# Optimization experiments

Measured on AMD Instinct MI355X. Metric: run time of the kernel, lower is better.

Reference implementation:

```python
import jax, jax.numpy as jnp
import numpy as np
from jax import lax

K = 10  # k_neighbors (k = min(k, N); N=1024 so k=10)


def setup_inputs() -> dict:
    key = jax.random.key(0)
    ks = jax.random.split(key, 6)
    B, N, M, D = 4, 1024, 8, 128
    PROJ, NC, OUT = 64, 10, 128
    x = jax.random.normal(ks[0], (B, N, M, D), dtype=jnp.float32)
    # Linear params (torch stores weight as [out, in])
    W_proj_w = jax.random.normal(ks[1], (PROJ, D), dtype=jnp.float32) / np.sqrt(D)
    W_proj_b = jnp.zeros((PROJ,), dtype=jnp.float32)
    C = jax.random.normal(ks[2], (NC, PROJ), dtype=jnp.float32) * np.sqrt(2.0 / (NC + PROJ))
    Theta_w = jax.random.normal(ks[3], (OUT, D), dtype=jnp.float32) / np.sqrt(D)
    Theta_b = jnp.zeros((OUT,), dtype=jnp.float32)
    return {"x": x, "W_proj_w": W_proj_w, "W_proj_b": W_proj_b, "C": C,
            "Theta_w": Theta_w, "Theta_b": Theta_b}


def _forward(x, W_proj_w, W_proj_b, C, Theta_w, Theta_b):
    B, N, M, D = x.shape
    BM = B * M
    x_flat = jnp.transpose(x, (0, 2, 1, 3)).reshape(BM, N, D)
    Z = x_flat @ W_proj_w.T + W_proj_b  # [BM, N, P]
    # squared euclidean pairwise distances (same topk ordering as cdist)
    sq = jnp.sum(Z * Z, axis=-1)  # [BM, N]
    d2 = sq[:, :, None] + sq[:, None, :] - 2.0 * jnp.einsum('bnp,bmp->bnm', Z, Z)
    _, idx = lax.top_k(-d2, K)  # k smallest distances -> [BM, N, K]
    # scatter 1.0 at neighbor indices
    b_ix = jnp.arange(BM)[:, None, None]
    r_ix = jnp.arange(N)[None, :, None]
    H_knn = jnp.zeros((BM, N, N), dtype=jnp.float32).at[b_ix, r_ix, idx].set(1.0)
    H_cluster = jax.nn.softmax(Z @ C.T, axis=-1)  # [BM, N, NC]
    H = jnp.concatenate([H_knn, H_cluster], axis=-1)  # [BM, N, N+NC]
    # hypergraph conv with degree normalization
    D_e = H.sum(axis=1)  # [BM, E]
    D_e_inv = jnp.where(D_e > 0, 1.0 / jnp.maximum(D_e, 1e-12), 0.0)
    D_v = H.sum(axis=2)  # [BM, N]
    D_v_inv_sqrt = jnp.where(D_v > 0, 1.0 / jnp.sqrt(jnp.maximum(D_v, 1e-12)), 0.0)
    X_trans = x_flat @ Theta_w.T + Theta_b  # [BM, N, F]
    out = D_v_inv_sqrt[:, :, None] * X_trans
    out = jnp.einsum('bne,bnf->bef', H, out)   # H^T @ out
    out = D_e_inv[:, :, None] * out
    out = jnp.einsum('bne,bef->bnf', H, out)   # H @ out
    out = D_v_inv_sqrt[:, :, None] * out
    out = jax.nn.elu(out)
    return jnp.transpose(out.reshape(B, M, N, -1), (0, 2, 1, 3))  # [B, N, M, F]


def reference(x, W_proj_w, W_proj_b, C, Theta_w, Theta_b):
    return _forward(x, W_proj_w, W_proj_b, C, Theta_w, Theta_b)
```

## Files before the change

### kernel.cpp

```cpp
#include <hip/hip_runtime.h>
#include <hip/hip_bf16.h>
#include <cstdint>
#include <cstddef>

#define BMC 32
#define NNODE 1024
#define DIN 128
#define PPROJ 64
#define NCLUS 10
#define FOUT 128
#define KNB 10

typedef _Float16 half8 __attribute__((ext_vector_type(8)));
typedef float f32x4 __attribute__((ext_vector_type(4)));

static const size_t OFF_Z    = 0;
static const size_t OFF_SQ   = 2097152;
static const size_t OFF_HC   = 2129920;
static const size_t OFF_IDX  = 2457600;
static const size_t OFF_CNT  = 2785280;
static const size_t OFF_FILL = 2818048;
static const size_t OFF_EC   = 2850816;
static const size_t OFF_DCV  = 2891776;
static const size_t OFF_OFFS = 2892096;
static const size_t OFF_ADJ  = 2924864;
static const size_t OFF_FLAG = 3252544;
static const size_t OFF_END  = 3252608;
static const size_t OFF_WPH  = OFF_EC;
static const size_t OFF_WPL  = OFF_EC +  4096;
static const size_t OFF_THH  = OFF_EC +  8192;
static const size_t OFF_THL  = OFF_EC + 16384;
static const int    ZERO2_N  = 41280;

__device__ __forceinline__ float bfu(unsigned int lo16) {
    return __uint_as_float(lo16 << 16);
}
__device__ __forceinline__ float bfhi(unsigned int w) {
    return __uint_as_float(w & 0xffff0000u);
}
__device__ __forceinline__ float ldf(const void* p, size_t i, bool isbf) {
    return isbf ? bfu((unsigned int)((const unsigned short*)p)[i])
                : ((const float*)p)[i];
}
__device__ __forceinline__ unsigned short f2bf(float v) {
    __hip_bfloat16 h = __float2bfloat16(v);
    return *(unsigned short*)&h;
}

__device__ __forceinline__ unsigned long long mkkey(float v, int col) {
    unsigned int bits = __float_as_uint(v);
    unsigned int s = bits ^ (0x80000000u | (unsigned int)((int)bits >> 31));
    return ((unsigned long long)s << 32) | (unsigned int)col;
}
__device__ __forceinline__ void kcas(unsigned long long &a, unsigned long long &b) {
    bool c = b < a;
    unsigned long long t = c ? b : a;
    b = c ? a : b;
    a = t;
}
__device__ __forceinline__ void kmin(unsigned long long &a, unsigned long long b) {
    a = (b < a) ? b : a;
}

__global__ __launch_bounds__(256) void k_probe(const unsigned int* __restrict__ xw,
                                               int* __restrict__ flag) {
    __shared__ int red[256];
    int t = threadIdx.x;
    int cnt = 0;
    for (int i = t; i < 1024; i += 256) {
        float b = bfu(xw[i] & 0xffffu);
        float ab = fabsf(b);
        if (ab > 9.5e-7f && ab < 1.0e6f) cnt++;
    }
    red[t] = cnt;
    __syncthreads();
    for (int off = 128; off > 0; off >>= 1) {
        if (t < off) red[t] += red[t + off];
        __syncthreads();
    }
    if (t == 0) flag[0] = (red[0] >= 700) ? 1 : 0;
}

__global__ __launch_bounds__(256) void k_split(const void* __restrict__ Wp,
                                               const void* __restrict__ Th,
                                               const int* __restrict__ flag,
                                               _Float16* __restrict__ WpH,
                                               _Float16* __restrict__ WpL,
                                               _Float16* __restrict__ ThH,
                                               _Float16* __restrict__ ThL,
                                               int* __restrict__ cntz) {
    const bool isbf = (flag[0] != 0);
    int i = blockIdx.x * 256 + threadIdx.x;
    cntz[i] = 0;
    if (i < 8192) cntz[i + 24576] = 0;
    if (i < 8192) {
        float v = ldf(Wp, i, isbf);
        _Float16 h = (_Float16)v;
        WpH[i] = h;
        WpL[i] = (_Float16)((v - (float)h) * 2048.0f);
    } else {
        int j = i - 8192;
        float v = ldf(Th, j, isbf);
        _Float16 h = (_Float16)v;
        ThH[j] = h;
        ThL[j] = (_Float16)((v - (float)h) * 2048.0f);
    }
}

__global__ __launch_bounds__(256) void k_proj(const void* __restrict__ x,
                                              const _Float16* __restrict__ WpH,
                                              const _Float16* __restrict__ WpL,
                                              const void* __restrict__ Wpb,
                                              const void* __restrict__ Cm,
                                              const int* __restrict__ flag,
                                              _Float16* __restrict__ Zh,
                                              _Float16* __restrict__ Zl,
                                              float* __restrict__ sqv,
                                              float* __restrict__ Hc) {
    __shared__ __align__(16) _Float16 wps[2][64][72];
    __shared__ __align__(16) _Float16 xsh[2][32][72];
    __shared__ float zs[32][68];
    __shared__ float cs[10][64];

    const bool isbf = (flag[0] != 0);
    int tid = threadIdx.x;
    int bi  = blockIdx.x;
    int bm  = bi >> 5;
    int n0  = (bi & 31) << 5;
    int b   = bm >> 3, m = bm & 7;

    int lane = tid & 63, wave = tid >> 6;
    int m16 = lane & 15, quad = lane >> 4;
    int rh = wave >> 1, ch = wave & 1;

    for (int e = tid; e < 640; e += 256) cs[e >> 6][e & 63] = ldf(Cm, e, isbf);

    f32x4 aH[2], aX[2];
#pragma unroll
    for (int t = 0; t < 2; ++t) {
        aH[t] = (f32x4){0.f, 0.f, 0.f, 0.f};
        aX[t] = (f32x4){0.f, 0.f, 0.f, 0.f};
    }

    for (int kc = 0; kc < 2; ++kc) {
        __syncthreads();
        for (int e = tid; e < 512; e += 256) {
            int p = e >> 3, c = e & 7;
            *(uint4*)&wps[0][p][c * 8] =
                *(const uint4*)(WpH + (size_t)p * 128 + kc * 64 + c * 8);
            *(uint4*)&wps[1][p][c * 8] =
                *(const uint4*)(WpL + (size_t)p * 128 + kc * 64 + c * 8);
        }
        for (int e = tid; e < 2048; e += 256) {
            int r = e >> 6, dk = e & 63;
            float v = ldf(x, (((size_t)b * NNODE + n0 + r) * 8 + m) * DIN + kc * 64 + dk, isbf);
            _Float16 h = (_Float16)v;
            xsh[0][r][dk] = h;
            xsh[1][r][dk] = (_Float16)((v - (float)h) * 2048.0f);
        }
        __syncthreads();
#pragma unroll
        for (int c32 = 0; c32 < 2; ++c32) {
            half8 Ah = *(const half8*)&xsh[0][rh * 16 + m16][c32 * 32 + quad * 8];
            half8 Al = *(const half8*)&xsh[1][rh * 16 + m16][c32 * 32 + quad * 8];
#pragma unroll
            for (int t = 0; t < 2; ++t) {
                int p = ch * 32 + t * 16 + m16;
                half8 Bh = *(const half8*)&wps[0][p][c32 * 32 + quad * 8];
                half8 Bl = *(const half8*)&wps[1][p][c32 * 32 + quad * 8];
                aH[t] = __builtin_amdgcn_mfma_f32_16x16x32_f16(Ah, Bh, aH[t], 0, 0, 0);
                aX[t] = __builtin_amdgcn_mfma_f32_16x16x32_f16(Al, Bh, aX[t], 0, 0, 0);
                aX[t] = __builtin_amdgcn_mfma_f32_16x16x32_f16(Ah, Bl, aX[t], 0, 0, 0);
            }
        }
    }

#pragma unroll
    for (int t = 0; t < 2; ++t) {
        int p = ch * 32 + t * 16 + m16;
        float bias = ldf(Wpb, p, isbf);
#pragma unroll
        for (int r = 0; r < 4; ++r) {
            int row = rh * 16 + quad * 4 + r;
            float v = aH[t][r] + aX[t][r] * (1.0f / 2048.0f) + bias;
            zs[row][p] = v;
            size_t off = ((size_t)bm * NNODE + n0 + row) * 64 + p;
            _Float16 h = (_Float16)v;
            Zh[off] = h;
            Zl[off] = (_Float16)((v - (float)h) * 2048.0f);
        }
    }
    __syncthreads();

    int row = tid >> 3, slot = tid & 7;
    int d0 = slot * 8;
    float sp = 0.f;
#pragma unroll
    for (int dd = 0; dd < 8; ++dd) { float z = zs[row][d0+dd]; sp += z * z; }
#pragma unroll
    for (int mm = 1; mm < 8; mm <<= 1) sp += __shfl_xor(sp, mm, 8);
    size_t g = (size_t)bm * NNODE + n0 + row;
    if (slot == 0) sqv[g] = sp;

    float sc[10];
#pragma unroll
    for (int c = 0; c < 10; ++c) {
        float pa = 0.f;
#pragma unroll
        for (int dd = 0; dd < 8; ++dd) pa += zs[row][d0+dd] * cs[c][d0+dd];
#pragma unroll
        for (int mm = 1; mm < 8; mm <<= 1) pa += __shfl_xor(pa, mm, 8);
        sc[c] = pa;
    }
    float mx = sc[0];
#pragma unroll
    for (int c = 1; c < 10; ++c) mx = fmaxf(mx, sc[c]);
    float ssum = 0.f;
#pragma unroll
    for (int c = 0; c < 10; ++c) { sc[c] = expf(sc[c] - mx); ssum += sc[c]; }
    float inv = 1.0f / ssum;
#pragma unroll
    for (int c = 0; c < 10; ++c)
        if ((c & 7) == slot) Hc[g * 10 + c] = sc[c] * inv;
}

__global__ __launch_bounds__(256) void k_theta(const void* __restrict__ x,
                                               const _Float16* __restrict__ ThH,
                                               const _Float16* __restrict__ ThL,
                                               const void* __restrict__ Thb,
                                               const int* __restrict__ flag,
                                               float* __restrict__ Xt) {
    __shared__ __align__(16) _Float16 ths[2][128][72];
    __shared__ __align__(16) _Float16 xsh[32][72];

    const bool isbf = (flag[0] != 0);
    int tid = threadIdx.x;
    int bi  = blockIdx.x;
    int bm  = bi >> 5;
    int n0  = (bi & 31) << 5;
    int b   = bm >> 3, m = bm & 7;

    int lane = tid & 63, wave = tid >> 6;
    int m16 = lane & 15, quad = lane >> 4;
    int rh = wave >> 1, ch = wave & 1;

    f32x4 aH[4], aX[4];
#pragma unroll
    for (int t = 0; t < 4; ++t) {
        aH[t] = (f32x4){0.f, 0.f, 0.f, 0.f};
        aX[t] = (f32x4){0.f, 0.f, 0.f, 0.f};
    }

    for (int kc = 0; kc < 2; ++kc) {
        __syncthreads();
        for (int e = tid; e < 1024; e += 256) {
            int f = e >> 3, c = e & 7;
            *(uint4*)&ths[0][f][c * 8] =
                *(const uint4*)(ThH + (size_t)f * 128 + kc * 64 + c * 8);
            *(uint4*)&ths[1][f][c * 8] =
                *(const uint4*)(ThL + (size_t)f * 128 + kc * 64 + c * 8);
        }
        for (int e = tid; e < 2048; e += 256) {
            int r = e >> 6, dk = e & 63;
            float v = ldf(x, (((size_t)b * NNODE + n0 + r) * 8 + m) * DIN + kc * 64 + dk, isbf);
            xsh[r][dk] = (_Float16)v;
        }
        __syncthreads();
#pragma unroll
        for (int c32 = 0; c32 < 2; ++c32) {
            half8 Ah = *(const half8*)&xsh[rh * 16 + m16][c32 * 32 + quad * 8];
#pragma unroll
            for (int t = 0; t < 4; ++t) {
                int f = ch * 64 + t * 16 + m16;
                half8 Bh = *(const half8*)&ths[0][f][c32 * 32 + quad * 8];
                half8 Bl = *(const half8*)&ths[1][f][c32 * 32 + quad * 8];
                aH[t] = __builtin_amdgcn_mfma_f32_16x16x32_f16(Ah, Bh, aH[t], 0, 0, 0);
                aX[t] = __builtin_amdgcn_mfma_f32_16x16x32_f16(Ah, Bl, aX[t], 0, 0, 0);
            }
        }
    }
#pragma unroll
    for (int t = 0; t < 4; ++t) {
        int f = ch * 64 + t * 16 + m16;
        float bias = ldf(Thb, f, isbf);
        size_t rb = (size_t)bm * NNODE + n0 + rh * 16 + quad * 4;
#pragma unroll
        for (int r = 0; r < 4; ++r) {
            Xt[(rb + r) * 128 + f] = aH[t][r] + aX[t][r] * (1.0f / 2048.0f) + bias;
        }
    }
}

__global__ __launch_bounds__(256) void k_topk(const _Float16* __restrict__ Zh,
                                              const _Float16* __restrict__ Zl,
                                              const float* __restrict__ sqv,
                                              int* __restrict__ idxo,
                                              int* __restrict__ cnt) {
    __shared__ __align__(16) _Float16 BH[64 * 72];
    __shared__ __align__(16) _Float16 BL[64 * 72];
    __shared__ float    ST[64 * 36];
    __shared__ float    sqt[64];

    int tid = threadIdx.x;
    int bi  = blockIdx.x;
    int bm  = bi >> 5;
    int n0  = (bi & 31) << 5;
    const _Float16* Zhb = Zh + (size_t)bm * NNODE * 64;
    const _Float16* Zlb = Zl + (size_t)bm * NNODE * 64;

    int lane = tid & 63, wave = tid >> 6;
    int m16 = lane & 15, quad = lane >> 4;

    half8 ah0, ah1, al0, al1, ah0b, ah1b, al0b, al1b;
    {
        size_t ab = (size_t)(n0 + m16) * 64 + quad * 8;
        ah0 = *(const half8*)(Zhb + ab);
        ah1 = *(const half8*)(Zhb + ab + 32);
        al0 = *(const half8*)(Zlb + ab);
        al1 = *(const half8*)(Zlb + ab + 32);
        size_t ab2 = ab + 16 * 64;
        ah0b = *(const half8*)(Zhb + ab2);
        ah1b = *(const half8*)(Zhb + ab2 + 32);
        al0b = *(const half8*)(Zlb + ab2);
        al1b = *(const half8*)(Zlb + ab2 + 32);
    }

    unsigned long long keys[10];
#pragma unroll
    for (int j = 0; j < 10; ++j) keys[j] = ~0ULL;

    int srow  = tid >> 3;
    int sslot = tid & 7;

    for (int t = 0; t < 16; ++t) {
        int j0 = t << 6;
        for (int e = tid; e < 512; e += 256) {
            int col = e >> 3, kc = e & 7;
            *(uint4*)&BH[col * 72 + kc * 8] =
                *(const uint4*)(Zhb + (size_t)(j0 + col) * 64 + kc * 8);
            *(uint4*)&BL[col * 72 + kc * 8] =
                *(const uint4*)(Zlb + (size_t)(j0 + col) * 64 + kc * 8);
        }
        if (tid < 64) sqt[tid] = sqv[(size_t)bm * NNODE + j0 + tid];
        __syncthreads();

        {
            int cl = wave * 16 + m16;
            const _Float16* pb = &BH[cl * 72 + quad * 8];
            const _Float16* pl = &BL[cl * 72 + quad * 8];
            half8 bh0 = *(const half8*)pb;
            half8 bh1 = *(const half8*)(pb + 32);
            half8 bl0 = *(const half8*)pl;
            half8 bl1 = *(const half8*)(pl + 32);
            float sqc = sqt[cl];

            f32x4 acc  = {0.f, 0.f, 0.f, 0.f};
            f32x4 accx = {0.f, 0.f, 0.f, 0.f};
            acc  = __builtin_amdgcn_mfma_f32_16x16x32_f16(ah0, bh0, acc, 0, 0, 0);
            acc  = __builtin_amdgcn_mfma_f32_16x16x32_f16(ah1, bh1, acc, 0, 0, 0);
            accx = __builtin_amdgcn_mfma_f32_16x16x32_f16(al0, bh0, accx, 0, 0, 0);
            accx = __builtin_amdgcn_mfma_f32_16x16x32_f16(ah0, bl0, accx, 0, 0, 0);
            accx = __builtin_amdgcn_mfma_f32_16x16x32_f16(al1, bh1, accx, 0, 0, 0);
            accx = __builtin_amdgcn_mfma_f32_16x16x32_f16(ah1, bl1, accx, 0, 0, 0);
            f32x4 sc;
#pragma unroll
            for (int r = 0; r < 4; ++r) {
                float g = acc[r] + accx[r] * (1.0f / 2048.0f);
                sc[r] = fmaf(-2.0f, g, sqc);
            }
            *(f32x4*)&ST[cl * 36 + quad * 4] = sc;

            f32x4 accB  = {0.f, 0.f, 0.f, 0.f};
            f32x4 accxB = {0.f, 0.f, 0.f, 0.f};
            accB  = __builtin_amdgcn_mfma_f32_16x16x32_f16(ah0b, bh0, accB, 0, 0, 0);
            accB  = __builtin_amdgcn_mfma_f32_16x16x32_f16(ah1b, bh1, accB, 0, 0, 0);
            accxB = __builtin_amdgcn_mfma_f32_16x16x32_f16(al0b, bh0, accxB, 0, 0, 0);
            accxB = __builtin_amdgcn_mfma_f32_16x16x32_f16(ah0b, bl0, accxB, 0, 0, 0);
            accxB = __builtin_amdgcn_mfma_f32_16x16x32_f16(al1b, bh1, accxB, 0, 0, 0);
            accxB = __builtin_amdgcn_mfma_f32_16x16x32_f16(ah1b, bl1, accxB, 0, 0, 0);
#pragma unroll
            for (int r = 0; r < 4; ++r) {
                float g = accB[r] + accxB[r] * (1.0f / 2048.0f);
                sc[r] = fmaf(-2.0f, g, sqc);
            }
            *(f32x4*)&ST[cl * 36 + 16 + quad * 4] = sc;
        }
        __syncthreads();

        unsigned long long b0 = mkkey(ST[(sslot     ) * 36 + srow], j0 + sslot);
        unsigned long long b1 = mkkey(ST[(sslot +  8) * 36 + srow], j0 + sslot + 8);
        unsigned long long b2 = mkkey(ST[(sslot + 16) * 36 + srow], j0 + sslot + 16);
        unsigned long long b3 = mkkey(ST[(sslot + 24) * 36 + srow], j0 + sslot + 24);
        unsigned long long b4 = mkkey(ST[(sslot + 32) * 36 + srow], j0 + sslot + 32);
        unsigned long long b5 = mkkey(ST[(sslot + 40) * 36 + srow], j0 + sslot + 40);
        unsigned long long b6 = mkkey(ST[(sslot + 48) * 36 + srow], j0 + sslot + 48);
        unsigned long long b7 = mkkey(ST[(sslot + 56) * 36 + srow], j0 + sslot + 56);

        kcas(b0, b1); kcas(b2, b3); kcas(b4, b5); kcas(b6, b7);
        kcas(b0, b2); kcas(b1, b3); kcas(b4, b6); kcas(b5, b7);
        kcas(b1, b2); kcas(b5, b6);
        kcas(b0, b4); kcas(b1, b5); kcas(b2, b6); kcas(b3, b7);
        kcas(b2, b4); kcas(b3, b5);
        kcas(b1, b2); kcas(b3, b4); kcas(b5, b6);

        kmin(keys[2], b7); kmin(keys[3], b6); kmin(keys[4], b5); kmin(keys[5], b4);
        kmin(keys[6], b3); kmin(keys[7], b2); kmin(keys[8], b1); kmin(keys[9], b0);

        kcas(keys[0], keys[8]); kcas(keys[1], keys[9]);
        kcas(keys[2], keys[6]); kcas(keys[3], keys[7]);
        kcas(keys[4], keys[8]); kcas(keys[5], keys[9]);
        kcas(keys[2], keys[4]); kcas(keys[3], keys[5]);
        kcas(keys[6], keys[8]); kcas(keys[7], keys[9]);
        kcas(keys[0], keys[1]); kcas(keys[2], keys[3]);
        kcas(keys[4], keys[5]); kcas(keys[6], keys[7]); kcas(keys[8], keys[9]);
    }

    size_t gr = (size_t)bm * NNODE + n0 + srow;
    for (int it = 0; it < 10; ++it) {
        unsigned long long mine = keys[0];
        unsigned long long best = mine;
#pragma unroll
        for (int mm = 1; mm < 8; mm <<= 1) {
            unsigned long long o = __shfl_xor(best, mm, 8);
            if (o < best) best = o;
        }
        if (best == mine) {
#pragma unroll
            for (int j = 0; j < 9; ++j) keys[j] = keys[j+1];
            keys[9] = ~0ULL;
            int col = (int)(best & 0xFFFFFFFFu);
            idxo[gr * KNB + it] = col;
            atomicAdd(&cnt[bm * NNODE + col], 1);
        }
    }
}

__global__ __launch_bounds__(256) void k_csr(const int* __restrict__ cnt,
                                             const int* __restrict__ idxb,
                                             int* __restrict__ offs,
                                             int* __restrict__ adj) {
    __shared__ int part[256];
    __shared__ int fillL[1024];
    int bm = blockIdx.x, t = threadIdx.x;
    int base = bm * 1024 + t * 4;
    int c0 = cnt[base], c1 = cnt[base+1], c2 = cnt[base+2], c3 = cnt[base+3];
    int ps = c0 + c1 + c2 + c3;
    part[t] = ps;
    __syncthreads();
    for (int off = 1; off < 256; off <<= 1) {
        int add = (t >= off) ? part[t - off] : 0;
        __syncthreads();
        part[t] += add;
        __syncthreads();
    }
    int e0 = part[t] - ps;
    int gb = bm * (NNODE * KNB);
    int o0 = gb + e0, o1 = o0 + c0, o2 = o1 + c1, o3 = o2 + c2;
    offs[base]   = o0;
    offs[base+1] = o1;
    offs[base+2] = o2;
    offs[base+3] = o3;
    fillL[t*4]   = o0;
    fillL[t*4+1] = o1;
    fillL[t*4+2] = o2;
    fillL[t*4+3] = o3;
    __syncthreads();
    int ibase = bm * (NNODE * KNB);
    for (int e = t; e < NNODE * KNB; e += 256) {
        int eidx = idxb[ibase + e];
        int pos = atomicAdd(&fillL[eidx], 1);
        adj[pos] = (bm << 10) + (e / 10);
    }
}

__global__ __launch_bounds__(256) void k_edge(const float* __restrict__ Xt,
                                              const int* __restrict__ offs,
                                              const int* __restrict__ cnt,
                                              const int* __restrict__ adj,
                                              unsigned short* __restrict__ Ek,
                                              float* __restrict__ EcZ) {
    int tid = threadIdx.x;
    int bi  = blockIdx.x;
    {
        int zi = bi * 256 + tid;
        if (zi < ZERO2_N) EcZ[zi] = 0.0f;
    }
    int swz = (bi & 7) * 512 + (bi >> 3);
    int e = swz * 8 + (tid >> 5);
    int l = tid & 31;
    int start = offs[e];
    int num = cnt[e];
    float4 acc = {0.f, 0.f, 0.f, 0.f};
    if (num > 0) {
        int nm1 = num - 1;
        int gidx[16];
#pragma unroll
        for (int j = 0; j < 16; ++j) {
            int jj = (j < nm1) ? j : nm1;
            gidx[j] = adj[start + jj];
        }
#pragma unroll
        for (int j = 0; j < 16; ++j) {
            float4 a = *(const float4*)(Xt + (size_t)gidx[j] * 128 + l * 4);
            float w = (j < num) ? 1.0f : 0.0f;
            acc.x = fmaf(w, a.x, acc.x);
            acc.y = fmaf(w, a.y, acc.y);
            acc.z = fmaf(w, a.z, acc.z);
            acc.w = fmaf(w, a.w, acc.w);
        }
        int i = 16;
        for (; i + 1 < num; i += 2) {
            int g0 = adj[start + i];
            int g1 = adj[start + i + 1];
            float4 a = *(const float4*)(Xt + (size_t)g0 * 128 + l * 4);
            float4 b = *(const float4*)(Xt + (size_t)g1 * 128 + l * 4);
            acc.x += a.x + b.x; acc.y += a.y + b.y;
            acc.z += a.z + b.z; acc.w += a.w + b.w;
        }
        if (i < num) {
            int g0 = adj[start + i];
            float4 a = *(const float4*)(Xt + (size_t)g0 * 128 + l * 4);
            acc.x += a.x; acc.y += a.y; acc.z += a.z; acc.w += a.w;
        }
    }
    float scale = (num > 0) ? 1.0f / (float)num : 0.0f;
    ushort4 o;
    o.x = f2bf(acc.x * scale);
    o.y = f2bf(acc.y * scale);
    o.z = f2bf(acc.z * scale);
    o.w = f2bf(acc.w * scale);
    *(ushort4*)(Ek + (size_t)e * 128 + l * 4) = o;
}

__global__ __launch_bounds__(256) void k_clus(const float* __restrict__ Xt,
                                              const float* __restrict__ Hc,
                                              float* __restrict__ Ec,
                                              float* __restrict__ Dcv) {
    __shared__ float hcs[128][12];
    int tid = threadIdx.x;
    int bm = blockIdx.x >> 3;
    int ch = blockIdx.x & 7;
    int n0 = ch * 128;

    for (int e = tid; e < 1280; e += 256) {
        int r = e / 10, c = e - r * 10;
        hcs[r][c] = Hc[((size_t)bm * NNODE + n0 + r) * 10 + c];
    }
    __syncthreads();

    int f = tid & 127;
    int h = tid >> 7;
    int c0 = h * 5;
    float acc[5]  = {0.f,0.f,0.f,0.f,0.f};
    float dacc[5] = {0.f,0.f,0.f,0.f,0.f};
#pragma unroll 2
    for (int n = 0; n < 128; ++n) {
        float xv = Xt[((size_t)bm * NNODE + n0 + n) * 128 + f];
#pragma unroll
        for (int j = 0; j < 5; ++j) {
            float hv = hcs[n][c0 + j];
            acc[j]  = fmaf(hv, xv, acc[j]);
            dacc[j] += hv;
        }
    }
#pragma unroll
    for (int j = 0; j < 5; ++j)
        atomicAdd(&Ec[((size_t)bm * 10 + c0 + j) * 128 + f], acc[j]);
    if (f == 0) {
#pragma unroll
        for (int j = 0; j < 5; ++j) atomicAdd(&Dcv[bm * 10 + c0 + j], dacc[j]);
    }
}

__global__ __launch_bounds__(256) void k_final(const unsigned short* __restrict__ Ek,
                                               const float* __restrict__ Ec,
                                               const float* __restrict__ Hc,
                                               const float* __restrict__ Dcv,
                                               const int* __restrict__ idxb,
                                               float* __restrict__ out) {
    int tid = threadIdx.x;
    int bi  = blockIdx.x;
    int swz = (bi & 7) * 512 + (bi >> 3);
    int g = swz * 8 + (tid >> 5);
    int l = tid & 31;
    int bm = g >> 10, n = g & 1023;
    const int* ip = idxb + (size_t)g * 10;
    const unsigned short* ekb = Ek + ((size_t)bm << 10) * 128 + l * 4;

    float4 acc = {0.f, 0.f, 0.f, 0.f};
#pragma unroll
    for (int k = 0; k < 10; k += 2) {
        int e0 = ip[k], e1 = ip[k + 1];
        ushort4 u0 = *(const ushort4*)(ekb + (size_t)e0 * 128);
        ushort4 u1 = *(const ushort4*)(ekb + (size_t)e1 * 128);
        acc.x += bfu(u0.x) + bfu(u1.x);
        acc.y += bfu(u0.y) + bfu(u1.y);
        acc.z += bfu(u0.z) + bfu(u1.z);
        acc.w += bfu(u0.w) + bfu(u1.w);
    }
    const float* hp  = Hc + (size_t)g * 10;
    const float* dcp = Dcv + (size_t)bm * 10;
    const float* ecp = Ec + (size_t)bm * 10 * 128 + l * 4;
#pragma unroll
    for (int c = 0; c < 10; ++c) {
        float d  = dcp[c];
        float hv = (d > 0.f) ? hp[c] / d : 0.f;
        float4 ec = *(const float4*)(ecp + c * 128);
        acc.x += hv * ec.x; acc.y += hv * ec.y;
        acc.z += hv * ec.z; acc.w += hv * ec.w;
    }
    float4 r;
    r.x = acc.x * (1.0f / 11.0f);
    r.y = acc.y * (1.0f / 11.0f);
    r.z = acc.z * (1.0f / 11.0f);
    r.w = acc.w * (1.0f / 11.0f);
    r.x = (r.x > 0.f) ? r.x : expm1f(r.x);
    r.y = (r.y > 0.f) ? r.y : expm1f(r.y);
    r.z = (r.z > 0.f) ? r.z : expm1f(r.z);
    r.w = (r.w > 0.f) ? r.w : expm1f(r.w);
    int b = bm >> 3, m = bm & 7;
    *(float4*)(out + (((size_t)b * NNODE + n) * 8 + m) * 128 + l * 4) = r;
}

extern "C" void kernel_launch(void* const* d_in, const int* in_sizes, int n_in,
                              void* d_out, int out_size, void* d_ws, size_t ws_size,
                              hipStream_t stream) {
    const void* x   = d_in[0];
    const void* Wp  = d_in[1];
    const void* Wpb = d_in[2];
    const void* Cm  = d_in[3];
    const void* Th  = d_in[4];
    const void* Thb = d_in[5];
    float* ws = (float*)d_ws;

    if (ws_size < OFF_END * sizeof(float)) return;

    _Float16* Zh = (_Float16*)(ws + OFF_Z);
    _Float16* Zl = (_Float16*)(ws + OFF_Z + 1048576);
    float* sqv  = ws + OFF_SQ;
    float* Hc   = ws + OFF_HC;
    int*   idxb = (int*)(ws + OFF_IDX);
    int*   cnt  = (int*)(ws + OFF_CNT);
    float* Ec   = ws + OFF_EC;
    float* Dcv  = ws + OFF_DCV;
    int*   offs = (int*)(ws + OFF_OFFS);
    int*   adj  = (int*)(ws + OFF_ADJ);
    int*   flag = (int*)(ws + OFF_FLAG);
    _Float16* WpH = (_Float16*)(ws + OFF_WPH);
    _Float16* WpL = (_Float16*)(ws + OFF_WPL);
    _Float16* ThH = (_Float16*)(ws + OFF_THH);
    _Float16* ThL = (_Float16*)(ws + OFF_THL);
    unsigned short* Ek = (unsigned short*)(ws + OFF_Z);
    float* Xt  = (float*)d_out;
    float* out = (float*)d_out;

    k_probe <<<1,    256, 0, stream>>>((const unsigned int*)x, flag);
    k_split <<<96,   256, 0, stream>>>(Wp, Th, flag, WpH, WpL, ThH, ThL, cnt);
    k_proj  <<<1024, 256, 0, stream>>>(x, WpH, WpL, Wpb, Cm, flag, Zh, Zl, sqv, Hc);
    k_topk  <<<1024, 256, 0, stream>>>(Zh, Zl, sqv, idxb, cnt);
    k_csr   <<<32,   256, 0, stream>>>(cnt, idxb, offs, adj);
    k_theta <<<1024, 256, 0, stream>>>(x, ThH, ThL, Thb, flag, Xt);
    k_edge  <<<4096, 256, 0, stream>>>(Xt, offs, cnt, adj, Ek, Ec);
    k_clus  <<<256,  256, 0, stream>>>(Xt, Hc, Ec, Dcv);
    k_final <<<4096, 256, 0, stream>>>(Ek, Ec, Hc, Dcv, idxb, out);
}
```

Baseline: 273.3 us.

## Load topk B tiles directly from global, split clus blocks, batch final gathers

The topk kernel stops staging Z high/low tiles and squared norms through shared memory. Each wave now loads its column fragments straight from global memory, relying on cache reuse, and only ST stays in LDS. The cluster aggregation kernel splits rows into 32-node chunks across four times as many blocks, which raises parallelism but also the atomic count. The final kernel issues all ten neighbour gathers up front to increase memory-level parallelism.

```diff
diff --git a/kernel.cpp b/kernel.cpp
--- a/kernel.cpp
+++ b/kernel.cpp
@@ -296,10 +296,7 @@
                                               const float* __restrict__ sqv,
                                               int* __restrict__ idxo,
                                               int* __restrict__ cnt) {
-    __shared__ __align__(16) _Float16 BH[64 * 72];
-    __shared__ __align__(16) _Float16 BL[64 * 72];
-    __shared__ float    ST[64 * 36];
-    __shared__ float    sqt[64];
+    __shared__ float ST[64 * 36];
 
     int tid = threadIdx.x;
     int bi  = blockIdx.x;
@@ -307,6 +304,7 @@
     int n0  = (bi & 31) << 5;
     const _Float16* Zhb = Zh + (size_t)bm * NNODE * 64;
     const _Float16* Zlb = Zl + (size_t)bm * NNODE * 64;
+    const float*    sqb = sqv + (size_t)bm * NNODE;
 
     int lane = tid & 63, wave = tid >> 6;
     int m16 = lane & 15, quad = lane >> 4;
@@ -334,25 +332,15 @@
 
     for (int t = 0; t < 16; ++t) {
         int j0 = t << 6;
-        for (int e = tid; e < 512; e += 256) {
-            int col = e >> 3, kc = e & 7;
-            *(uint4*)&BH[col * 72 + kc * 8] =
-                *(const uint4*)(Zhb + (size_t)(j0 + col) * 64 + kc * 8);
-            *(uint4*)&BL[col * 72 + kc * 8] =
-                *(const uint4*)(Zlb + (size_t)(j0 + col) * 64 + kc * 8);
-        }
-        if (tid < 64) sqt[tid] = sqv[(size_t)bm * NNODE + j0 + tid];
-        __syncthreads();
-
         {
             int cl = wave * 16 + m16;
-            const _Float16* pb = &BH[cl * 72 + quad * 8];
-            const _Float16* pl = &BL[cl * 72 + quad * 8];
+            const _Float16* pb = Zhb + (size_t)(j0 + cl) * 64 + quad * 8;
+            const _Float16* pl = Zlb + (size_t)(j0 + cl) * 64 + quad * 8;
             half8 bh0 = *(const half8*)pb;
             half8 bh1 = *(const half8*)(pb + 32);
             half8 bl0 = *(const half8*)pl;
             half8 bl1 = *(const half8*)(pl + 32);
-            float sqc = sqt[cl];
+            float sqc = sqb[j0 + cl];
 
             f32x4 acc  = {0.f, 0.f, 0.f, 0.f};
             f32x4 accx = {0.f, 0.f, 0.f, 0.f};
@@ -413,6 +401,7 @@
         kcas(keys[6], keys[8]); kcas(keys[7], keys[9]);
         kcas(keys[0], keys[1]); kcas(keys[2], keys[3]);
         kcas(keys[4], keys[5]); kcas(keys[6], keys[7]); kcas(keys[8], keys[9]);
+        __syncthreads();
     }
 
     size_t gr = (size_t)bm * NNODE + n0 + srow;
@@ -536,13 +525,13 @@
                                               const float* __restrict__ Hc,
                                               float* __restrict__ Ec,
                                               float* __restrict__ Dcv) {
-    __shared__ float hcs[128][12];
+    __shared__ float hcs[32][12];
     int tid = threadIdx.x;
-    int bm = blockIdx.x >> 3;
-    int ch = blockIdx.x & 7;
-    int n0 = ch * 128;
-
-    for (int e = tid; e < 1280; e += 256) {
+    int bm = blockIdx.x >> 5;
+    int ch = blockIdx.x & 31;
+    int n0 = ch * 32;
+
+    for (int e = tid; e < 320; e += 256) {
         int r = e / 10, c = e - r * 10;
         hcs[r][c] = Hc[((size_t)bm * NNODE + n0 + r) * 10 + c];
     }
@@ -553,8 +542,8 @@
     int c0 = h * 5;
     float acc[5]  = {0.f,0.f,0.f,0.f,0.f};
     float dacc[5] = {0.f,0.f,0.f,0.f,0.f};
-#pragma unroll 2
-    for (int n = 0; n < 128; ++n) {
+#pragma unroll 4
+    for (int n = 0; n < 32; ++n) {
         float xv = Xt[((size_t)bm * NNODE + n0 + n) * 128 + f];
 #pragma unroll
         for (int j = 0; j < 5; ++j) {
@@ -587,17 +576,29 @@
     const int* ip = idxb + (size_t)g * 10;
     const unsigned short* ekb = Ek + ((size_t)bm << 10) * 128 + l * 4;
 
-    float4 acc = {0.f, 0.f, 0.f, 0.f};
-#pragma unroll
-    for (int k = 0; k < 10; k += 2) {
-        int e0 = ip[k], e1 = ip[k + 1];
-        ushort4 u0 = *(const ushort4*)(ekb + (size_t)e0 * 128);
-        ushort4 u1 = *(const ushort4*)(ekb + (size_t)e1 * 128);
-        acc.x += bfu(u0.x) + bfu(u1.x);
-        acc.y += bfu(u0.y) + bfu(u1.y);
-        acc.z += bfu(u0.z) + bfu(u1.z);
-        acc.w += bfu(u0.w) + bfu(u1.w);
-    }
+    int e0 = ip[0], e1 = ip[1], e2 = ip[2], e3 = ip[3], e4 = ip[4];
+    int e5 = ip[5], e6 = ip[6], e7 = ip[7], e8 = ip[8], e9 = ip[9];
+    ushort4 u0 = *(const ushort4*)(ekb + (size_t)e0 * 128);
+    ushort4 u1 = *(const ushort4*)(ekb + (size_t)e1 * 128);
+    ushort4 u2 = *(const ushort4*)(ekb + (size_t)e2 * 128);
+    ushort4 u3 = *(const ushort4*)(ekb + (size_t)e3 * 128);
+    ushort4 u4 = *(const ushort4*)(ekb + (size_t)e4 * 128);
+    ushort4 u5 = *(const ushort4*)(ekb + (size_t)e5 * 128);
+    ushort4 u6 = *(const ushort4*)(ekb + (size_t)e6 * 128);
+    ushort4 u7 = *(const ushort4*)(ekb + (size_t)e7 * 128);
+    ushort4 u8 = *(const ushort4*)(ekb + (size_t)e8 * 128);
+    ushort4 u9 = *(const ushort4*)(ekb + (size_t)e9 * 128);
+
+    float4 acc;
+    acc.x = bfu(u0.x) + bfu(u1.x) + bfu(u2.x) + bfu(u3.x) + bfu(u4.x)
+          + bfu(u5.x) + bfu(u6.x) + bfu(u7.x) + bfu(u8.x) + bfu(u9.x);
+    acc.y = bfu(u0.y) + bfu(u1.y) + bfu(u2.y) + bfu(u3.y) + bfu(u4.y)
+          + bfu(u5.y) + bfu(u6.y) + bfu(u7.y) + bfu(u8.y) + bfu(u9.y);
+    acc.z = bfu(u0.z) + bfu(u1.z) + bfu(u2.z) + bfu(u3.z) + bfu(u4.z)
+          + bfu(u5.z) + bfu(u6.z) + bfu(u7.z) + bfu(u8.z) + bfu(u9.z);
+    acc.w = bfu(u0.w) + bfu(u1.w) + bfu(u2.w) + bfu(u3.w) + bfu(u4.w)
+          + bfu(u5.w) + bfu(u6.w) + bfu(u7.w) + bfu(u8.w) + bfu(u9.w);
+
     const float* hp  = Hc + (size_t)g * 10;
     const float* dcp = Dcv + (size_t)bm * 10;
     const float* ecp = Ec + (size_t)bm * 10 * 128 + l * 4;
@@ -661,6 +662,6 @@
     k_csr   <<<32,   256, 0, stream>>>(cnt, idxb, offs, adj);
     k_theta <<<1024, 256, 0, stream>>>(x, ThH, ThL, Thb, flag, Xt);
     k_edge  <<<4096, 256, 0, stream>>>(Xt, offs, cnt, adj, Ek, Ec);
-    k_clus  <<<256,  256, 0, stream>>>(Xt, Hc, Ec, Dcv);
+    k_clus  <<<1024, 256, 0, stream>>>(Xt, Hc, Ec, Dcv);
     k_final <<<4096, 256, 0, stream>>>(Ek, Ec, Hc, Dcv, idxb, out);
 }
```

Result: no change. 277.7 us (+1.6%).
